# Optimization experiments

Hardware: AMD Instinct MI355X
Metric: run time of the kernel (lower is better)

Reference implementation:

```python
import jax, jax.numpy as jnp
import numpy as np

VOCAB = 65
N_EMBD = 32
BLOCK = 8
N_HEADS = 4
HEAD = N_EMBD // N_HEADS  # 8
SQRT_C = float(N_EMBD) ** 0.5  # faithful bug: scores are MULTIPLIED by sqrt(n_embd)


def setup_inputs() -> dict:
    key = jax.random.key(0)
    ks = jax.random.split(key, 12)
    B, T = 65536, 8
    idx = jax.random.randint(ks[0], (B, T), 0, VOCAB, dtype=jnp.int64 if jax.config.jax_enable_x64 else jnp.int32)
    targets = jax.random.randint(ks[1], (B, T), 0, VOCAB, dtype=idx.dtype)
    s = 1.0 / np.sqrt(N_EMBD)
    return {
        "idx": idx,
        "targets": targets,
        "tok_emb": jax.random.normal(ks[2], (VOCAB, N_EMBD), jnp.float32),
        "pos_emb": jax.random.normal(ks[3], (BLOCK, N_EMBD), jnp.float32),
        # per-head Q/K/V projections stacked: [n_heads, n_embd, head_size]
        "Wq": jax.random.normal(ks[4], (N_HEADS, N_EMBD, HEAD), jnp.float32) * s,
        "Wk": jax.random.normal(ks[5], (N_HEADS, N_EMBD, HEAD), jnp.float32) * s,
        "Wv": jax.random.normal(ks[6], (N_HEADS, N_EMBD, HEAD), jnp.float32) * s,
        "W_mlp": jax.random.normal(ks[7], (N_EMBD, N_EMBD), jnp.float32) * s,
        "b_mlp": jnp.zeros((N_EMBD,), jnp.float32),
        "W_lm": jax.random.normal(ks[8], (N_EMBD, VOCAB), jnp.float32) * s,
        "b_lm": jnp.zeros((VOCAB,), jnp.float32),
    }


def reference(idx, targets, tok_emb, pos_emb, Wq, Wk, Wv, W_mlp, b_mlp, W_lm, b_lm):
    B, T = idx.shape
    x = tok_emb[idx] + pos_emb[:T]                       # [B,T,C]
    q = jnp.einsum('btc,hcd->bhtd', x, Wq)               # [B,H,T,D]
    k = jnp.einsum('btc,hcd->bhtd', x, Wk)
    v = jnp.einsum('btc,hcd->bhtd', x, Wv)
    wei = jnp.einsum('bhtd,bhsd->bhts', q, k) * SQRT_C   # faithful: * C**0.5
    tril = jnp.tril(jnp.ones((T, T), bool))
    wei = jnp.where(tril, wei, -jnp.inf)
    wei = jax.nn.softmax(wei, axis=-1)
    out = jnp.einsum('bhts,bhsd->bhtd', wei, v)          # [B,H,T,D]
    x = out.transpose(0, 2, 1, 3).reshape(B, T, N_EMBD)  # concat heads
    x = jax.nn.relu(x @ W_mlp + b_mlp)                   # MLP
    logits = x @ W_lm + b_lm                             # [B,T,V]
    logits = logits.reshape(B * T, VOCAB)
    logp = jax.nn.log_softmax(logits, axis=-1)
    tgt = targets.reshape(B * T)
    loss = -jnp.take_along_axis(logp, tgt[:, None], axis=-1).mean()
    return logits, loss
```

## Files before the change

### kernel.cpp

```cpp
#include <hip/hip_runtime.h>
#include <hip/hip_bf16.h>

#define VOCAB   65
#define SQRT_C  5.656854249492381f
#define BATCHES 65536
#define ROWS    (BATCHES * 8)
#define TABSZ   (8 * VOCAB * 32)
#define PAIRS   (BATCHES / 2)
#define NBLOCKS 2048
#define NWAVES  (NBLOCKS * 4)

typedef __attribute__((ext_vector_type(8))) short  short8;
typedef __attribute__((ext_vector_type(4))) float  float4v;

__device__ __forceinline__ void wave_fence() {
    __asm__ volatile("s_waitcnt lgkmcnt(0)" ::: "memory");
}
__device__ __forceinline__ short bfbits(float f) {
    __hip_bfloat16 h = __float2bfloat16(f);
    return *reinterpret_cast<short*>(&h);
}

__global__ void qkv_table_kernel(const float* __restrict__ tok_emb,
                                 const float* __restrict__ pos_emb,
                                 const float* __restrict__ Wq,
                                 const float* __restrict__ Wk,
                                 const float* __restrict__ Wv,
                                 float* __restrict__ qtab,
                                 float* __restrict__ ktab,
                                 float* __restrict__ vtab) {
    int o = blockIdx.x * 256 + threadIdx.x;
    if (o >= 3 * TABSZ) return;
    int table = o / TABSZ;
    int r = o - table * TABSZ;
    int pair = r >> 5;
    int cd = r & 31;
    int t = pair / VOCAB;
    int tok = pair - t * VOCAB;
    int h = cd >> 3, d = cd & 7;
    const float* W = (table == 0) ? Wq : (table == 1) ? Wk : Wv;
    float acc = 0.f;
    #pragma unroll
    for (int c = 0; c < 32; ++c) {
        float xc = tok_emb[tok * 32 + c] + pos_emb[t * 32 + c];
        acc += xc * W[h * 256 + c * 8 + d];
    }
    float* tab = (table == 0) ? qtab : (table == 1) ? ktab : vtab;
    tab[r] = acc;
}

__global__ __launch_bounds__(256) void fused_kernel(
        const int* __restrict__ idx, const int* __restrict__ targets,
        const float* __restrict__ qtab, const float* __restrict__ ktab,
        const float* __restrict__ vtab,
        const float* __restrict__ W_mlp,
        const float* __restrict__ b_mlp,
        const float* __restrict__ W_lm,
        const float* __restrict__ b_lm,
        float* __restrict__ out_logits,
        float* __restrict__ loss_acc) {
    __shared__ __align__(16) float sK[4][544];
    __shared__ __align__(16) float sV[4][544];
    __shared__ __align__(16) unsigned short sX3[4][640];

    const int tid = threadIdx.x;
    const int w = tid >> 6, l = tid & 63;
    const int q4 = l >> 4;
    const int n  = l & 15;
    const int t  = l & 7, b2 = (l >> 3) & 1, h = q4;

    short8 wmf[2], wlf[4], wlf4;
    #pragma unroll
    for (int c = 0; c < 2; ++c)
        #pragma unroll
        for (int j = 0; j < 8; ++j)
            wmf[c][j] = bfbits(W_mlp[(q4 * 8 + j) * 32 + c * 16 + n]);
    #pragma unroll
    for (int c = 0; c < 4; ++c)
        #pragma unroll
        for (int j = 0; j < 8; ++j)
            wlf[c][j] = bfbits(W_lm[(q4 * 8 + j) * VOCAB + c * 16 + n]);
    #pragma unroll
    for (int j = 0; j < 8; ++j)
        wlf4[j] = (n == 0) ? bfbits(W_lm[(q4 * 8 + j) * VOCAB + 64]) : (short)0;
    float bmc[2], blc[4];
    #pragma unroll
    for (int c = 0; c < 2; ++c) bmc[c] = b_mlp[c * 16 + n];
    #pragma unroll
    for (int c = 0; c < 4; ++c) blc[c] = b_lm[c * 16 + n];
    const float bl64 = b_lm[64];
    const float4v zf = {0.f, 0.f, 0.f, 0.f};

    float loss_local = 0.f;

    for (int pb = blockIdx.x * 4 + w; pb < PAIRS; pb += NWAVES) {
        int tokv = 0, tgv = 0;
        if (l < 16) { tokv = idx[pb * 16 + l]; tgv = targets[pb * 16 + l]; }

        #pragma unroll
        for (int half = 0; half < 2; ++half) {
            int c = l + half * 64;
            int d2 = c & 1, s = (c >> 1) & 7, grp = c >> 4;
            int b2g = grp & 1, hg = grp >> 1;
            int tok_s = __shfl(tokv, b2g * 8 + s);
            int gaddr = (s * VOCAB + tok_s) * 32 + hg * 8 + d2 * 4;
            int laddr = grp * 68 + s * 8 + d2 * 4;
            *(float4*)(&sK[w][laddr]) = *(const float4*)(ktab + gaddr);
            *(float4*)(&sV[w][laddr]) = *(const float4*)(vtab + gaddr);
        }
        int tok_t = __shfl(tokv, b2 * 8 + t);
        const float* qp = qtab + (t * VOCAB + tok_t) * 32 + h * 8;
        const float4 q0 = *(const float4*)(qp);
        const float4 q1 = *(const float4*)(qp + 4);
        wave_fence();

        const float* kb = &sK[w][(h * 2 + b2) * 68];
        const float* vb = &sV[w][(h * 2 + b2) * 68];
        float sc[8], m = -1e30f;
        #pragma unroll
        for (int s = 0; s < 8; ++s) {
            float4 k0 = *(const float4*)(kb + s * 8);
            float4 k1 = *(const float4*)(kb + s * 8 + 4);
            float d = q0.x * k0.x + q0.y * k0.y + q0.z * k0.z + q0.w * k0.w
                    + q1.x * k1.x + q1.y * k1.y + q1.z * k1.z + q1.w * k1.w;
            d *= SQRT_C;
            sc[s] = d;
            if (s <= t) m = fmaxf(m, d);
        }
        float p[8], sum = 0.f;
        #pragma unroll
        for (int s = 0; s < 8; ++s) {
            p[s] = (s <= t) ? __expf(sc[s] - m) : 0.f;
            sum += p[s];
        }
        float inv = 1.f / sum;
        float o[8];
        #pragma unroll
        for (int d = 0; d < 8; ++d) o[d] = 0.f;
        #pragma unroll
        for (int s = 0; s < 8; ++s) {
            float4 v0 = *(const float4*)(vb + s * 8);
            float4 v1 = *(const float4*)(vb + s * 8 + 4);
            o[0] += p[s] * v0.x; o[1] += p[s] * v0.y; o[2] += p[s] * v0.z; o[3] += p[s] * v0.w;
            o[4] += p[s] * v1.x; o[5] += p[s] * v1.y; o[6] += p[s] * v1.z; o[7] += p[s] * v1.w;
        }
        short8 a2;
        #pragma unroll
        for (int d = 0; d < 8; ++d) a2[d] = bfbits(o[d] * inv);

        float4v d0 = __builtin_amdgcn_mfma_f32_16x16x32_bf16(a2, wmf[0], zf, 0, 0, 0);
        float4v d1 = __builtin_amdgcn_mfma_f32_16x16x32_bf16(a2, wmf[1], zf, 0, 0, 0);
        #pragma unroll
        for (int i = 0; i < 4; ++i) {
            int row = q4 * 4 + i;
            sX3[w][row * 40 + n]      = (unsigned short)bfbits(fmaxf(d0[i] + bmc[0], 0.f));
            sX3[w][row * 40 + 16 + n] = (unsigned short)bfbits(fmaxf(d1[i] + bmc[1], 0.f));
        }
        wave_fence();
        short8 a3 = *(const short8*)(&sX3[w][n * 40 + q4 * 8]);

        int tgn = __shfl(tgv, n);
        short8 b6;
        #pragma unroll
        for (int j = 0; j < 8; ++j) b6[j] = bfbits(W_lm[(q4 * 8 + j) * VOCAB + tgn]);
        float btg = b_lm[tgn];

        float4v Lc[4];
        #pragma unroll
        for (int c = 0; c < 4; ++c)
            Lc[c] = __builtin_amdgcn_mfma_f32_16x16x32_bf16(a3, wlf[c], zf, 0, 0, 0);
        float4v L64 = __builtin_amdgcn_mfma_f32_16x16x32_bf16(a3, wlf4, zf, 0, 0, 0);
        float4v Ltg = __builtin_amdgcn_mfma_f32_16x16x32_bf16(a3, b6, zf, 0, 0, 0);

        size_t rb = (size_t)pb * 16;
        float part[4] = {0.f, 0.f, 0.f, 0.f};
        #pragma unroll
        for (int c = 0; c < 4; ++c) {
            #pragma unroll
            for (int i = 0; i < 4; ++i) {
                float Lv = Lc[c][i] + blc[c];
                out_logits[(rb + q4 * 4 + i) * VOCAB + c * 16 + n] = Lv;
                part[i] += __expf(Lv);
            }
        }
        if (n == 0) {
            #pragma unroll
            for (int i = 0; i < 4; ++i) {
                float Lv = L64[i] + bl64;
                out_logits[(rb + q4 * 4 + i) * VOCAB + 64] = Lv;
                part[i] += __expf(Lv);
            }
        }
        #pragma unroll
        for (int off = 1; off < 16; off <<= 1) {
            #pragma unroll
            for (int i = 0; i < 4; ++i) part[i] += __shfl_xor(part[i], off);
        }
        float lg = __logf(part[0]) + __logf(part[1]) + __logf(part[2]) + __logf(part[3]);
        if (n == 0) loss_local += lg;
        int rd = n - q4 * 4;
        float tval = (rd == 0) ? Ltg[0] : (rd == 1) ? Ltg[1] : (rd == 2) ? Ltg[2] : Ltg[3];
        if (rd >= 0 && rd <= 3) loss_local -= (tval + btg);
    }

    #pragma unroll
    for (int off = 1; off < 64; off <<= 1) loss_local += __shfl_xor(loss_local, off);
    if (l == 0) atomicAdd(loss_acc, loss_local);
}

__global__ void finalize_loss(const float* __restrict__ acc,
                              float* __restrict__ out) {
    out[0] = acc[0] * (1.f / (float)ROWS);
}

extern "C" void kernel_launch(void* const* d_in, const int* in_sizes, int n_in,
                              void* d_out, int out_size, void* d_ws, size_t ws_size,
                              hipStream_t stream) {
    const int* idx        = (const int*)d_in[0];
    const int* targets    = (const int*)d_in[1];
    const float* tok_emb  = (const float*)d_in[2];
    const float* pos_emb  = (const float*)d_in[3];
    const float* Wq       = (const float*)d_in[4];
    const float* Wk       = (const float*)d_in[5];
    const float* Wv       = (const float*)d_in[6];
    const float* W_mlp    = (const float*)d_in[7];
    const float* b_mlp    = (const float*)d_in[8];
    const float* W_lm     = (const float*)d_in[9];
    const float* b_lm     = (const float*)d_in[10];
    float* out            = (float*)d_out;

    float* ws       = (float*)d_ws;
    float* loss_ptr = ws;
    float* qtab     = ws + 16;
    float* ktab     = qtab + TABSZ;
    float* vtab     = ktab + TABSZ;

    hipMemsetAsync(loss_ptr, 0, sizeof(float), stream);

    qkv_table_kernel<<<(3 * TABSZ + 255) / 256, 256, 0, stream>>>(
        tok_emb, pos_emb, Wq, Wk, Wv, qtab, ktab, vtab);

    fused_kernel<<<NBLOCKS, 256, 0, stream>>>(
        idx, targets, qtab, ktab, vtab, W_mlp, b_mlp, W_lm, b_lm, out, loss_ptr);

    finalize_loss<<<1, 1, 0, stream>>>(loss_ptr, out + (size_t)ROWS * VOCAB);
}
```

Before: 321.4 us.

## Read K/V tables directly, fold sqrt(C) into Q table, select target logit in-register

```diff
diff --git a/kernel.cpp b/kernel.cpp
--- a/kernel.cpp
+++ b/kernel.cpp
@@ -12,6 +12,7 @@
 
 typedef __attribute__((ext_vector_type(8))) short  short8;
 typedef __attribute__((ext_vector_type(4))) float  float4v;
+typedef __attribute__((ext_vector_type(4))) int    intv4;
 
 __device__ __forceinline__ void wave_fence() {
     __asm__ volatile("s_waitcnt lgkmcnt(0)" ::: "memory");
@@ -19,6 +20,11 @@
 __device__ __forceinline__ short bfbits(float f) {
     __hip_bfloat16 h = __float2bfloat16(f);
     return *reinterpret_cast<short*>(&h);
+}
+__device__ __forceinline__ float dot8(const float4 a0, const float4 a1,
+                                      const float4 b0, const float4 b1) {
+    return a0.x*b0.x + a0.y*b0.y + a0.z*b0.z + a0.w*b0.w
+         + a1.x*b1.x + a1.y*b1.y + a1.z*b1.z + a1.w*b1.w;
 }
 
 __global__ void qkv_table_kernel(const float* __restrict__ tok_emb,
@@ -45,11 +51,12 @@
         float xc = tok_emb[tok * 32 + c] + pos_emb[t * 32 + c];
         acc += xc * W[h * 256 + c * 8 + d];
     }
+    if (table == 0) acc *= SQRT_C;
     float* tab = (table == 0) ? qtab : (table == 1) ? ktab : vtab;
     tab[r] = acc;
 }
 
-__global__ __launch_bounds__(256) void fused_kernel(
+__global__ __launch_bounds__(256, 7) void fused_kernel(
         const int* __restrict__ idx, const int* __restrict__ targets,
         const float* __restrict__ qtab, const float* __restrict__ ktab,
         const float* __restrict__ vtab,
@@ -59,8 +66,6 @@
         const float* __restrict__ b_lm,
         float* __restrict__ out_logits,
         float* __restrict__ loss_acc) {
-    __shared__ __align__(16) float sK[4][544];
-    __shared__ __align__(16) float sV[4][544];
     __shared__ __align__(16) unsigned short sX3[4][640];
 
     const int tid = threadIdx.x;
@@ -94,36 +99,30 @@
     float loss_local = 0.f;
 
     for (int pb = blockIdx.x * 4 + w; pb < PAIRS; pb += NWAVES) {
-        int tokv = 0, tgv = 0;
-        if (l < 16) { tokv = idx[pb * 16 + l]; tgv = targets[pb * 16 + l]; }
-
-        #pragma unroll
-        for (int half = 0; half < 2; ++half) {
-            int c = l + half * 64;
-            int d2 = c & 1, s = (c >> 1) & 7, grp = c >> 4;
-            int b2g = grp & 1, hg = grp >> 1;
-            int tok_s = __shfl(tokv, b2g * 8 + s);
-            int gaddr = (s * VOCAB + tok_s) * 32 + hg * 8 + d2 * 4;
-            int laddr = grp * 68 + s * 8 + d2 * 4;
-            *(float4*)(&sK[w][laddr]) = *(const float4*)(ktab + gaddr);
-            *(float4*)(&sV[w][laddr]) = *(const float4*)(vtab + gaddr);
-        }
-        int tok_t = __shfl(tokv, b2 * 8 + t);
+        const int rbase = pb * 16;
+
+        const intv4 ta = __builtin_nontemporal_load(
+            (const intv4*)(idx + rbase + b2 * 8));
+        const intv4 tb = __builtin_nontemporal_load(
+            (const intv4*)(idx + rbase + b2 * 8) + 1);
+        const int tok_t = idx[rbase + b2 * 8 + t];
+        const intv4 tg = __builtin_nontemporal_load(
+            (const intv4*)(targets + rbase + q4 * 4));
+
         const float* qp = qtab + (t * VOCAB + tok_t) * 32 + h * 8;
         const float4 q0 = *(const float4*)(qp);
         const float4 q1 = *(const float4*)(qp + 4);
-        wave_fence();
-
-        const float* kb = &sK[w][(h * 2 + b2) * 68];
-        const float* vb = &sV[w][(h * 2 + b2) * 68];
+
+        const int toks[8] = {ta[0], ta[1], ta[2], ta[3],
+                             tb[0], tb[1], tb[2], tb[3]};
+
         float sc[8], m = -1e30f;
         #pragma unroll
         for (int s = 0; s < 8; ++s) {
-            float4 k0 = *(const float4*)(kb + s * 8);
-            float4 k1 = *(const float4*)(kb + s * 8 + 4);
-            float d = q0.x * k0.x + q0.y * k0.y + q0.z * k0.z + q0.w * k0.w
-                    + q1.x * k1.x + q1.y * k1.y + q1.z * k1.z + q1.w * k1.w;
-            d *= SQRT_C;
+            const float* kp = ktab + (s * VOCAB + toks[s]) * 32 + h * 8;
+            float4 k0 = *(const float4*)(kp);
+            float4 k1 = *(const float4*)(kp + 4);
+            float d = dot8(q0, q1, k0, k1);
             sc[s] = d;
             if (s <= t) m = fmaxf(m, d);
         }
@@ -134,15 +133,19 @@
             sum += p[s];
         }
         float inv = 1.f / sum;
+
         float o[8];
         #pragma unroll
         for (int d = 0; d < 8; ++d) o[d] = 0.f;
         #pragma unroll
         for (int s = 0; s < 8; ++s) {
-            float4 v0 = *(const float4*)(vb + s * 8);
-            float4 v1 = *(const float4*)(vb + s * 8 + 4);
-            o[0] += p[s] * v0.x; o[1] += p[s] * v0.y; o[2] += p[s] * v0.z; o[3] += p[s] * v0.w;
-            o[4] += p[s] * v1.x; o[5] += p[s] * v1.y; o[6] += p[s] * v1.z; o[7] += p[s] * v1.w;
+            const float* vp = vtab + (s * VOCAB + toks[s]) * 32 + h * 8;
+            float4 v0 = *(const float4*)(vp);
+            float4 v1 = *(const float4*)(vp + 4);
+            o[0] += p[s] * v0.x; o[1] += p[s] * v0.y;
+            o[2] += p[s] * v0.z; o[3] += p[s] * v0.w;
+            o[4] += p[s] * v1.x; o[5] += p[s] * v1.y;
+            o[6] += p[s] * v1.z; o[7] += p[s] * v1.w;
         }
         short8 a2;
         #pragma unroll
@@ -159,36 +162,32 @@
         wave_fence();
         short8 a3 = *(const short8*)(&sX3[w][n * 40 + q4 * 8]);
 
-        int tgn = __shfl(tgv, n);
-        short8 b6;
-        #pragma unroll
-        for (int j = 0; j < 8; ++j) b6[j] = bfbits(W_lm[(q4 * 8 + j) * VOCAB + tgn]);
-        float btg = b_lm[tgn];
-
         float4v Lc[4];
         #pragma unroll
         for (int c = 0; c < 4; ++c)
             Lc[c] = __builtin_amdgcn_mfma_f32_16x16x32_bf16(a3, wlf[c], zf, 0, 0, 0);
         float4v L64 = __builtin_amdgcn_mfma_f32_16x16x32_bf16(a3, wlf4, zf, 0, 0, 0);
-        float4v Ltg = __builtin_amdgcn_mfma_f32_16x16x32_bf16(a3, b6, zf, 0, 0, 0);
-
-        size_t rb = (size_t)pb * 16;
+
         float part[4] = {0.f, 0.f, 0.f, 0.f};
         #pragma unroll
         for (int c = 0; c < 4; ++c) {
             #pragma unroll
             for (int i = 0; i < 4; ++i) {
                 float Lv = Lc[c][i] + blc[c];
-                out_logits[(rb + q4 * 4 + i) * VOCAB + c * 16 + n] = Lv;
+                __builtin_nontemporal_store(
+                    Lv, out_logits + (size_t)(rbase + q4 * 4 + i) * VOCAB + c * 16 + n);
                 part[i] += __expf(Lv);
+                if (c * 16 + n == tg[i]) loss_local -= Lv;
             }
         }
         if (n == 0) {
             #pragma unroll
             for (int i = 0; i < 4; ++i) {
                 float Lv = L64[i] + bl64;
-                out_logits[(rb + q4 * 4 + i) * VOCAB + 64] = Lv;
+                __builtin_nontemporal_store(
+                    Lv, out_logits + (size_t)(rbase + q4 * 4 + i) * VOCAB + 64);
                 part[i] += __expf(Lv);
+                if (tg[i] == 64) loss_local -= Lv;
             }
         }
         #pragma unroll
@@ -196,11 +195,9 @@
             #pragma unroll
             for (int i = 0; i < 4; ++i) part[i] += __shfl_xor(part[i], off);
         }
-        float lg = __logf(part[0]) + __logf(part[1]) + __logf(part[2]) + __logf(part[3]);
-        if (n == 0) loss_local += lg;
-        int rd = n - q4 * 4;
-        float tval = (rd == 0) ? Ltg[0] : (rd == 1) ? Ltg[1] : (rd == 2) ? Ltg[2] : Ltg[3];
-        if (rd >= 0 && rd <= 3) loss_local -= (tval + btg);
+        if (n == 0)
+            loss_local += __logf(part[0]) + __logf(part[1])
+                        + __logf(part[2]) + __logf(part[3]);
     }
 
     #pragma unroll
```

Measured after the change: 472.7 us. 47.1% more time.
